# Kernel optimization log

Measured on AMD Instinct MI355X. Metric: run time of the kernel, lower is better.

The kernel has to match this reference:

```python
import jax, jax.numpy as jnp
import numpy as np

N_NODES = 100000
N_EDGES = 1600000
IN_CH = 128
HID_CH = 128
EMB_CH = 128
OUT_CH = 64


def _sage_conv(x, src, dst, W_l, b_l, W_r):
    # PyG SAGEConv (mean aggr): out = lin_l(mean_{j->i} x_j) + lin_r(x_i)
    n = x.shape[0]
    msg = x[src]                                             # [E, d] gather
    summed = jax.ops.segment_sum(msg, dst, num_segments=n)   # [N, d]
    cnt = jax.ops.segment_sum(jnp.ones((src.shape[0],), x.dtype), dst, num_segments=n)
    mean = summed / jnp.maximum(cnt, 1.0)[:, None]
    return mean @ W_l + b_l + x @ W_r


def setup_inputs() -> dict:
    key = jax.random.key(0)
    ks = jax.random.split(key, 10)
    x = jax.random.normal(ks[0], (N_NODES, IN_CH), dtype=jnp.float32)
    edge_index = jax.random.randint(ks[1], (2, N_EDGES), 0, N_NODES, dtype=jnp.int32)
    s1 = 1.0 / np.sqrt(IN_CH)
    s2 = 1.0 / np.sqrt(HID_CH)
    s3 = 1.0 / np.sqrt(EMB_CH)
    return {
        "x": x,
        "edge_index": edge_index,
        "W1l": jax.random.uniform(ks[2], (IN_CH, HID_CH), jnp.float32, -s1, s1),
        "b1": jnp.zeros((HID_CH,), jnp.float32),
        "W1r": jax.random.uniform(ks[3], (IN_CH, HID_CH), jnp.float32, -s1, s1),
        "W2l": jax.random.uniform(ks[4], (HID_CH, EMB_CH), jnp.float32, -s2, s2),
        "b2": jnp.zeros((EMB_CH,), jnp.float32),
        "W2r": jax.random.uniform(ks[5], (HID_CH, EMB_CH), jnp.float32, -s2, s2),
        "Wm": jax.random.uniform(ks[6], (EMB_CH, OUT_CH), jnp.float32, -s3, s3),
        "bm": jax.random.uniform(ks[7], (OUT_CH,), jnp.float32, -s3, s3),
    }


def reference(x, edge_index, W1l, b1, W1r, W2l, b2, W2r, Wm, bm):
    src, dst = edge_index[0], edge_index[1]
    h = jax.nn.relu(_sage_conv(x, src, dst, W1l, b1, W1r))
    emb = _sage_conv(h, src, dst, W2l, b2, W2r)
    out = emb @ Wm + bm
    # F.normalize(emb, p=2, dim=-1)
    norm = jnp.sqrt(jnp.sum(emb * emb, axis=-1, keepdims=True))
    emb_n = emb / jnp.maximum(norm, 1e-12)
    return out, emb_n
```

## Files before the change

### kernel.cpp

```cpp
#include <hip/hip_runtime.h>
#include <hip/hip_fp16.h>
#include <cstdint>
#include <cstddef>

#define N_NODES 100000
#define N_EDGES 1600000
#define BSH 6
#define BNODES 64
#define NB 1563
#define CHUNK 2048
#define LDK 136

typedef _Float16 f16x8 __attribute__((ext_vector_type(8)));
typedef float f32x4 __attribute__((ext_vector_type(4)));


__device__ __forceinline__ float h2f(ushort u) {
    __half_raw r;
    r.x = u;
    return __half2float(__half(r));
}

__device__ __forceinline__ ushort f2h(float f) {
    __half h = __float2half(f);
    return static_cast<__half_raw>(h).x;
}

__device__ __forceinline__ void acc4(float4& a, uint2 v) {
    a.x += h2f((ushort)(v.x & 0xffff));
    a.y += h2f((ushort)(v.x >> 16));
    a.z += h2f((ushort)(v.y & 0xffff));
    a.w += h2f((ushort)(v.y >> 16));
}


__global__ __launch_bounds__(256) void prep_all(
        const int* __restrict__ dst, int* __restrict__ bcnt, int E,
        const float* __restrict__ x, ushort* __restrict__ x_f16, int n4,
        const float* __restrict__ W1l, const float* __restrict__ W1r,
        const float* __restrict__ W2l, const float* __restrict__ W2r,
        const float* __restrict__ Wm,
        ushort* __restrict__ W1lP, ushort* __restrict__ W1rP,
        ushort* __restrict__ W2lP, ushort* __restrict__ W2rP,
        ushort* __restrict__ WmP) {
    int bid = blockIdx.x;
    if (bid < 256) {
        __shared__ int lh[NB];
        for (int i = threadIdx.x; i < NB; i += 256) lh[i] = 0;
        __syncthreads();
        for (int e = bid * 256 + threadIdx.x; e < E; e += 256 * 256)
            atomicAdd(&lh[dst[e] >> BSH], 1);
        __syncthreads();
        for (int i = threadIdx.x; i < NB; i += 256) {
            int v = lh[i];
            if (v) atomicAdd(&bcnt[i], v);
        }
    } else if (bid < 256 + 12500) {
        int i = (bid - 256) * 256 + threadIdx.x;
        if (i < n4) {
            float4 v = reinterpret_cast<const float4*>(x)[i];
            ushort4 o;
            o.x = f2h(v.x);
            o.y = f2h(v.y);
            o.z = f2h(v.z);
            o.w = f2h(v.w);
            reinterpret_cast<ushort4*>(x_f16)[i] = o;
        }
    } else {
        int t = (bid - (256 + 12500)) * 256 + threadIdx.x;
        if (t < 65536) {
            int wsel = t >> 14;
            int o = t & 16383;
            const float* srcs[4] = {W1l, W1r, W2l, W2r};
            ushort* dsts[4] = {W1lP, W1rP, W2lP, W2rP};
            int j = o & 7;
            int lane = (o >> 3) & 63;
            int kg = (o >> 9) & 3;
            int nf = o >> 11;
            int k = kg * 32 + (lane >> 4) * 8 + j;
            int c = nf * 16 + (lane & 15);
            dsts[wsel][o] = f2h(srcs[wsel][k * 128 + c]);
        } else if (t < 65536 + 8192) {
            int o = t - 65536;
            int j = o & 7;
            int lane = (o >> 3) & 63;
            int kg = (o >> 9) & 3;
            int nf = o >> 11;
            int k = kg * 32 + (lane >> 4) * 8 + j;
            int c = nf * 16 + (lane & 15);
            WmP[o] = f2h(Wm[k * 64 + c]);
        }
    }
}

__global__ void scan_buckets(const int* __restrict__ bcnt, int* __restrict__ boffs) {
    __shared__ int sdata[256];
    int tid = threadIdx.x;
    int v[8];
    int s = 0;
#pragma unroll
    for (int i = 0; i < 8; i++) {
        int idx = tid * 8 + i;
        v[i] = (idx < NB) ? bcnt[idx] : 0;
        s += v[i];
    }
    sdata[tid] = s;
    __syncthreads();
    int acc = s;
    for (int off = 1; off < 256; off <<= 1) {
        int t = (tid >= off) ? sdata[tid - off] : 0;
        __syncthreads();
        acc += t;
        sdata[tid] = acc;
        __syncthreads();
    }
    int excl = acc - s;
#pragma unroll
    for (int i = 0; i < 8; i++) {
        int idx = tid * 8 + i;
        if (idx < NB) boffs[idx] = excl;
        excl += v[i];
    }
}

__global__ void bucket_scatter(const int* __restrict__ src, const int* __restrict__ dst,
                               const int* __restrict__ boffs, int* __restrict__ gcur,
                               uint* __restrict__ bedges, int E) {
    __shared__ int lh[NB];
    __shared__ int lbase[NB];
    int nwg = gridDim.x;
    int chunk = (E + nwg - 1) / nwg;
    int e0 = blockIdx.x * chunk;
    int e1 = e0 + chunk;
    if (e1 > E) e1 = E;
    for (int i = threadIdx.x; i < NB; i += 256) lh[i] = 0;
    __syncthreads();
    for (int e = e0 + threadIdx.x; e < e1; e += 256)
        atomicAdd(&lh[dst[e] >> BSH], 1);
    __syncthreads();
    for (int i = threadIdx.x; i < NB; i += 256) {
        int v = lh[i];
        lbase[i] = v ? (boffs[i] + atomicAdd(&gcur[i], v)) : 0;
    }
    __syncthreads();
    for (int i = threadIdx.x; i < NB; i += 256) lh[i] = 0;
    __syncthreads();
    int e = e0 + threadIdx.x;
#pragma unroll 1
    for (; e + 3 * 256 < e1; e += 4 * 256) {
        int d0 = dst[e + 0 * 256], s0 = src[e + 0 * 256];
        int d1 = dst[e + 1 * 256], s1 = src[e + 1 * 256];
        int d2 = dst[e + 2 * 256], s2 = src[e + 2 * 256];
        int d3 = dst[e + 3 * 256], s3 = src[e + 3 * 256];
        int b0 = d0 >> BSH, b1 = d1 >> BSH, b2 = d2 >> BSH, b3 = d3 >> BSH;
        int r0 = atomicAdd(&lh[b0], 1);
        int r1 = atomicAdd(&lh[b1], 1);
        int r2 = atomicAdd(&lh[b2], 1);
        int r3 = atomicAdd(&lh[b3], 1);
        bedges[lbase[b0] + r0] = ((uint)(d0 & (BNODES - 1)) << 17) | (uint)s0;
        bedges[lbase[b1] + r1] = ((uint)(d1 & (BNODES - 1)) << 17) | (uint)s1;
        bedges[lbase[b2] + r2] = ((uint)(d2 & (BNODES - 1)) << 17) | (uint)s2;
        bedges[lbase[b3] + r3] = ((uint)(d3 & (BNODES - 1)) << 17) | (uint)s3;
    }
    for (; e < e1; e += 256) {
        int d = dst[e];
        int b = d >> BSH;
        int r = atomicAdd(&lh[b], 1);
        bedges[lbase[b] + r] = ((uint)(d & (BNODES - 1)) << 17) | (uint)src[e];
    }
}


__global__ __launch_bounds__(512) void aggregate_bucket(
        const ushort* __restrict__ F, const uint* __restrict__ bedges,
        const int* __restrict__ boffs, const int* __restrict__ bcnt,
        ushort* __restrict__ out, int n) {
    int b = blockIdx.x;
    int beg = boffs[b];
    int m = bcnt[b];
    int node0 = b << BSH;
    int nNodes = n - node0;
    if (nNodes > BNODES) nNodes = BNODES;
    __shared__ uint ls[CHUNK];
    __shared__ int lh[BNODES];
    __shared__ int lofs[BNODES];
    __shared__ int pcnt[BNODES];
    int tid = threadIdx.x;
    int wid = tid >> 6;
    int lane = tid & 63;
    int hw = lane >> 5;
    int cl = lane & 31;

    float4 acc[8];
#pragma unroll
    for (int i = 0; i < 8; i++) acc[i] = make_float4(0.f, 0.f, 0.f, 0.f);
    if (tid < BNODES) pcnt[tid] = 0;

    for (int base = 0; base < m; base += CHUNK) {
        int mm = m - base;
        if (mm > CHUNK) mm = CHUNK;
        __syncthreads();
        if (tid < BNODES) lh[tid] = 0;
        __syncthreads();
        for (int i = tid; i < mm; i += 512)
            atomicAdd(&lh[bedges[beg + base + i] >> 17], 1);
        __syncthreads();
        if (tid < BNODES) {
            int v = lh[tid];
            int s = v;
#pragma unroll
            for (int off = 1; off < 64; off <<= 1) {
                int t = __shfl_up(s, off);
                if (lane >= off) s += t;
            }
            lofs[tid] = s - v;
            pcnt[tid] += v;
            lh[tid] = 0;
        }
        __syncthreads();
        for (int i = tid; i < mm; i += 512) {
            uint p = bedges[beg + base + i];
            int k = p >> 17;
            int r = atomicAdd(&lh[k], 1);
            ls[lofs[k] + r] = p;
        }
        __syncthreads();
#pragma unroll
        for (int ki = 0; ki < 8; ki++) {
            int k = wid * 8 + ki;
            int s0 = lofs[k];
            int ck = lh[k];
            int j = hw;
            for (; j + 6 < ck; j += 8) {
                uint p0 = ls[s0 + j + 0] & 0x1FFFFu;
                uint p1 = ls[s0 + j + 2] & 0x1FFFFu;
                uint p2 = ls[s0 + j + 4] & 0x1FFFFu;
                uint p3 = ls[s0 + j + 6] & 0x1FFFFu;
                uint2 v0 = *reinterpret_cast<const uint2*>(F + (size_t)p0 * 128 + cl * 4);
                uint2 v1 = *reinterpret_cast<const uint2*>(F + (size_t)p1 * 128 + cl * 4);
                uint2 v2 = *reinterpret_cast<const uint2*>(F + (size_t)p2 * 128 + cl * 4);
                uint2 v3 = *reinterpret_cast<const uint2*>(F + (size_t)p3 * 128 + cl * 4);
                acc4(acc[ki], v0);
                acc4(acc[ki], v1);
                acc4(acc[ki], v2);
                acc4(acc[ki], v3);
            }
            for (; j < ck; j += 2) {
                uint p = ls[s0 + j] & 0x1FFFFu;
                uint2 v = *reinterpret_cast<const uint2*>(F + (size_t)p * 128 + cl * 4);
                acc4(acc[ki], v);
            }
        }
    }
    __syncthreads();
#pragma unroll
    for (int ki = 0; ki < 8; ki++) {
        acc[ki].x += __shfl_xor(acc[ki].x, 32);
        acc[ki].y += __shfl_xor(acc[ki].y, 32);
        acc[ki].z += __shfl_xor(acc[ki].z, 32);
        acc[ki].w += __shfl_xor(acc[ki].w, 32);
    }
    if (hw == 0) {
#pragma unroll
        for (int ki = 0; ki < 8; ki++) {
            int k = wid * 8 + ki;
            if (k < nNodes) {
                float inv = 1.0f / fmaxf((float)pcnt[k], 1.0f);
                uint2 o;
                o.x = (uint)f2h(acc[ki].x * inv) | ((uint)f2h(acc[ki].y * inv) << 16);
                o.y = (uint)f2h(acc[ki].z * inv) | ((uint)f2h(acc[ki].w * inv) << 16);
                *reinterpret_cast<uint2*>(out + (size_t)(node0 + k) * 128 + cl * 4) = o;
            }
        }
    }
}


__global__ __launch_bounds__(256) void gemm1(
        const ushort* __restrict__ A1, const ushort* __restrict__ W1lP,
        const ushort* __restrict__ A2, const ushort* __restrict__ W1rP,
        const float* __restrict__ b1, ushort* __restrict__ h_f16, int n) {
    __shared__ ushort ht[64 * LDK];
    int wid = threadIdx.x >> 6;
    int lane = threadIdx.x & 63;
    int row0 = blockIdx.x * 64 + wid * 16;
    int fr = lane & 15;
    int ko = (lane >> 4) * 8;
    int arow = row0 + fr;
    if (arow >= n) arow = n - 1;

    f32x4 acc[8];
#pragma unroll
    for (int nf = 0; nf < 8; nf++) acc[nf] = (f32x4)0.f;

    for (int seg = 0; seg < 2; ++seg) {
        const ushort* A = seg ? A2 : A1;
        const ushort* WP = seg ? W1rP : W1lP;
#pragma unroll
        for (int kg = 0; kg < 4; kg++) {
            f16x8 av = *reinterpret_cast<const f16x8*>(A + (size_t)arow * 128 + kg * 32 + ko);
#pragma unroll
            for (int nf = 0; nf < 8; nf++) {
                f16x8 bv = *reinterpret_cast<const f16x8*>(WP + (nf * 4 + kg) * 512 + lane * 8);
                acc[nf] = __builtin_amdgcn_mfma_f32_16x16x32_f16(av, bv, acc[nf], 0, 0, 0);
            }
        }
    }

    int crow = (lane >> 4) * 4;
    int ccol = lane & 15;
#pragma unroll
    for (int reg = 0; reg < 4; reg++) {
        int lrow = wid * 16 + crow + reg;
#pragma unroll
        for (int nf = 0; nf < 8; nf++) {
            float v = acc[nf][reg] + b1[nf * 16 + ccol];
            v = fmaxf(v, 0.f);
            ht[lrow * LDK + nf * 16 + ccol] = f2h(v);
        }
    }
    __syncthreads();

#pragma unroll
    for (int i = 0; i < 16; i++) {
        int row = wid * 16 + i;
        int grow = blockIdx.x * 64 + row;
        if (grow < n) {
            reinterpret_cast<uint*>(h_f16 + (size_t)grow * 128)[lane] =
                reinterpret_cast<const uint*>(&ht[row * LDK])[lane];
        }
    }
}


__global__ __launch_bounds__(256) void gemm2(
        const ushort* __restrict__ A1, const ushort* __restrict__ W2lP,
        const ushort* __restrict__ A2, const ushort* __restrict__ W2rP,
        const float* __restrict__ b2, const ushort* __restrict__ WmP,
        const float* __restrict__ bm, float* __restrict__ outp,
        float* __restrict__ embn, int n) {
    __shared__ ushort et[64 * LDK];
    __shared__ float rnorm[64];
    int wid = threadIdx.x >> 6;
    int lane = threadIdx.x & 63;
    int row0 = blockIdx.x * 64 + wid * 16;
    int fr = lane & 15;
    int ko = (lane >> 4) * 8;
    int arow = row0 + fr;
    if (arow >= n) arow = n - 1;

    f32x4 acc[8];
#pragma unroll
    for (int nf = 0; nf < 8; nf++) acc[nf] = (f32x4)0.f;

    for (int seg = 0; seg < 2; ++seg) {
        const ushort* A = seg ? A2 : A1;
        const ushort* WP = seg ? W2rP : W2lP;
#pragma unroll
        for (int kg = 0; kg < 4; kg++) {
            f16x8 av = *reinterpret_cast<const f16x8*>(A + (size_t)arow * 128 + kg * 32 + ko);
#pragma unroll
            for (int nf = 0; nf < 8; nf++) {
                f16x8 bv = *reinterpret_cast<const f16x8*>(WP + (nf * 4 + kg) * 512 + lane * 8);
                acc[nf] = __builtin_amdgcn_mfma_f32_16x16x32_f16(av, bv, acc[nf], 0, 0, 0);
            }
        }
    }

    int crow = (lane >> 4) * 4;
    int ccol = lane & 15;
#pragma unroll
    for (int reg = 0; reg < 4; reg++) {
        float vv[8];
        float ss = 0.f;
#pragma unroll
        for (int nf = 0; nf < 8; nf++) {
            float v = acc[nf][reg] + b2[nf * 16 + ccol];
            vv[nf] = v;
            ss += v * v;
        }
        ss += __shfl_xor(ss, 1);
        ss += __shfl_xor(ss, 2);
        ss += __shfl_xor(ss, 4);
        ss += __shfl_xor(ss, 8);
        float inv = 1.0f / fmaxf(sqrtf(ss), 1e-12f);
        int lrow = wid * 16 + crow + reg;
#pragma unroll
        for (int nf = 0; nf < 8; nf++)
            et[lrow * LDK + nf * 16 + ccol] = f2h(vv[nf]);
        if (ccol == 0) rnorm[lrow] = inv;
    }
    __syncthreads();

#pragma unroll
    for (int i = 0; i < 16; i++) {
        int row = wid * 16 + i;
        int grow = blockIdx.x * 64 + row;
        if (grow < n) {
            float inv = rnorm[row];
            ushort2 e = reinterpret_cast<const ushort2*>(&et[row * LDK])[lane];
            float2 o;
            o.x = h2f(e.x) * inv;
            o.y = h2f(e.y) * inv;
            reinterpret_cast<float2*>(embn + (size_t)grow * 128)[lane] = o;
        }
    }

    f32x4 acc2[4];
#pragma unroll
    for (int nf = 0; nf < 4; nf++) acc2[nf] = (f32x4)0.f;
#pragma unroll
    for (int kg = 0; kg < 4; kg++) {
        f16x8 av = *reinterpret_cast<const f16x8*>(&et[(wid * 16 + fr) * LDK + kg * 32 + ko]);
#pragma unroll
        for (int nf = 0; nf < 4; nf++) {
            f16x8 bv = *reinterpret_cast<const f16x8*>(WmP + (nf * 4 + kg) * 512 + lane * 8);
            acc2[nf] = __builtin_amdgcn_mfma_f32_16x16x32_f16(av, bv, acc2[nf], 0, 0, 0);
        }
    }
#pragma unroll
    for (int reg = 0; reg < 4; reg++) {
        int grow = row0 + crow + reg;
        if (grow < n) {
#pragma unroll
            for (int nf = 0; nf < 4; nf++)
                outp[(size_t)grow * 64 + nf * 16 + ccol] = acc2[nf][reg] + bm[nf * 16 + ccol];
        }
    }
}


extern "C" void kernel_launch(void* const* d_in, const int* in_sizes, int n_in,
                              void* d_out, int out_size, void* d_ws, size_t ws_size,
                              hipStream_t stream) {
    const float* x   = (const float*)d_in[0];
    const int*   ei  = (const int*)d_in[1];
    const float* W1l = (const float*)d_in[2];
    const float* b1  = (const float*)d_in[3];
    const float* W1r = (const float*)d_in[4];
    const float* W2l = (const float*)d_in[5];
    const float* b2  = (const float*)d_in[6];
    const float* W2r = (const float*)d_in[7];
    const float* Wm  = (const float*)d_in[8];
    const float* bm  = (const float*)d_in[9];

    const int N = N_NODES, E = N_EDGES;
    const int* src = ei;
    const int* dst = ei + E;

    char* ws = (char*)d_ws;
    int* bcnt  = (int*)ws;  ws += sizeof(int) * NB;
    int* boffs = (int*)ws;  ws += sizeof(int) * NB;
    int* gcur  = (int*)ws;  ws += sizeof(int) * NB;
    uintptr_t p0 = ((uintptr_t)ws + 255) & ~(uintptr_t)255;
    uint* bedges = (uint*)p0;
    uintptr_t p1 = ((uintptr_t)(bedges + N_EDGES) + 255) & ~(uintptr_t)255;
    ushort* mean_f16 = (ushort*)p1;
    ushort* x_f16    = mean_f16 + (size_t)N * 128;
    ushort* h_f16    = x_f16 + (size_t)N * 128;
    ushort* W1lP     = h_f16 + (size_t)N * 128;
    ushort* W1rP     = W1lP + 128 * 128;
    ushort* W2lP     = W1rP + 128 * 128;
    ushort* W2rP     = W2lP + 128 * 128;
    ushort* WmP      = W2rP + 128 * 128;

    float* outp = (float*)d_out;
    float* embn = outp + (size_t)N * 64;

    hipMemsetAsync(bcnt, 0, sizeof(int) * NB, stream);
    hipMemsetAsync(gcur, 0, sizeof(int) * NB, stream);

    int n4 = N * 128 / 4;
    int prep_blocks = 256 + 12500 + 288;
    prep_all<<<prep_blocks, 256, 0, stream>>>(dst, bcnt, E, x, x_f16, n4,
                                              W1l, W1r, W2l, W2r, Wm,
                                              W1lP, W1rP, W2lP, W2rP, WmP);
    scan_buckets<<<1, 256, 0, stream>>>(bcnt, boffs);
    bucket_scatter<<<256, 256, 0, stream>>>(src, dst, boffs, gcur, bedges, E);

    int gblk = (N + 63) / 64;

    aggregate_bucket<<<NB, 512, 0, stream>>>(x_f16, bedges, boffs, bcnt, mean_f16, N);
    gemm1<<<gblk, 256, 0, stream>>>(mean_f16, W1lP, x_f16, W1rP, b1, h_f16, N);

    aggregate_bucket<<<NB, 512, 0, stream>>>(h_f16, bedges, boffs, bcnt, mean_f16, N);
    gemm2<<<gblk, 256, 0, stream>>>(mean_f16, W2lP, h_f16, W2rP, b2,
                                    WmP, bm, outp, embn, N);
}
```

Baseline: 287.9 us.

## Presort edges into per-node CSR once and aggregate with feature-sliced blocks

Adds a sort_buckets kernel that turns the bucketed edge list into a per-node CSR (sorted sources, offsets, counts) once, so both aggregation passes reuse it instead of re-sorting each bucket in shared memory. The aggregation kernel now splits the 128 features into four 32-column slices, one block per slice, with 16-lane groups reading 4-byte pieces. This removes the repeated in-block histogram, atomics and syncs and raises block count, but each source row is now fetched as four narrow 64-byte pieces spread across four blocks, and it adds an extra kernel plus workspace.

```diff
diff --git a/kernel.cpp b/kernel.cpp
--- a/kernel.cpp
+++ b/kernel.cpp
@@ -8,7 +8,6 @@
 #define BSH 6
 #define BNODES 64
 #define NB 1563
-#define CHUNK 2048
 #define LDK 136
 
 typedef _Float16 f16x8 __attribute__((ext_vector_type(8)));
@@ -24,13 +23,6 @@
 __device__ __forceinline__ ushort f2h(float f) {
     __half h = __float2half(f);
     return static_cast<__half_raw>(h).x;
-}
-
-__device__ __forceinline__ void acc4(float4& a, uint2 v) {
-    a.x += h2f((ushort)(v.x & 0xffff));
-    a.y += h2f((ushort)(v.x >> 16));
-    a.z += h2f((ushort)(v.y & 0xffff));
-    a.w += h2f((ushort)(v.y >> 16));
 }
 
 
@@ -171,106 +163,89 @@
 }
 
 
-__global__ __launch_bounds__(512) void aggregate_bucket(
-        const ushort* __restrict__ F, const uint* __restrict__ bedges,
-        const int* __restrict__ boffs, const int* __restrict__ bcnt,
-        ushort* __restrict__ out, int n) {
+__global__ __launch_bounds__(256) void sort_buckets(
+        const uint* __restrict__ bedges, const int* __restrict__ boffs,
+        const int* __restrict__ bcnt, uint* __restrict__ srcs_sorted,
+        int* __restrict__ noffs, int* __restrict__ ncnt, int n) {
+    __shared__ int lh[BNODES];
+    __shared__ int lofs[BNODES];
     int b = blockIdx.x;
     int beg = boffs[b];
     int m = bcnt[b];
     int node0 = b << BSH;
-    int nNodes = n - node0;
-    if (nNodes > BNODES) nNodes = BNODES;
-    __shared__ uint ls[CHUNK];
-    __shared__ int lh[BNODES];
-    __shared__ int lofs[BNODES];
-    __shared__ int pcnt[BNODES];
     int tid = threadIdx.x;
-    int wid = tid >> 6;
-    int lane = tid & 63;
-    int hw = lane >> 5;
-    int cl = lane & 31;
-
-    float4 acc[8];
-#pragma unroll
-    for (int i = 0; i < 8; i++) acc[i] = make_float4(0.f, 0.f, 0.f, 0.f);
-    if (tid < BNODES) pcnt[tid] = 0;
-
-    for (int base = 0; base < m; base += CHUNK) {
-        int mm = m - base;
-        if (mm > CHUNK) mm = CHUNK;
-        __syncthreads();
-        if (tid < BNODES) lh[tid] = 0;
-        __syncthreads();
-        for (int i = tid; i < mm; i += 512)
-            atomicAdd(&lh[bedges[beg + base + i] >> 17], 1);
-        __syncthreads();
-        if (tid < BNODES) {
-            int v = lh[tid];
-            int s = v;
-#pragma unroll
-            for (int off = 1; off < 64; off <<= 1) {
-                int t = __shfl_up(s, off);
-                if (lane >= off) s += t;
-            }
-            lofs[tid] = s - v;
-            pcnt[tid] += v;
-            lh[tid] = 0;
-        }
-        __syncthreads();
-        for (int i = tid; i < mm; i += 512) {
-            uint p = bedges[beg + base + i];
-            int k = p >> 17;
-            int r = atomicAdd(&lh[k], 1);
-            ls[lofs[k] + r] = p;
-        }
-        __syncthreads();
-#pragma unroll
-        for (int ki = 0; ki < 8; ki++) {
-            int k = wid * 8 + ki;
-            int s0 = lofs[k];
-            int ck = lh[k];
-            int j = hw;
-            for (; j + 6 < ck; j += 8) {
-                uint p0 = ls[s0 + j + 0] & 0x1FFFFu;
-                uint p1 = ls[s0 + j + 2] & 0x1FFFFu;
-                uint p2 = ls[s0 + j + 4] & 0x1FFFFu;
-                uint p3 = ls[s0 + j + 6] & 0x1FFFFu;
-                uint2 v0 = *reinterpret_cast<const uint2*>(F + (size_t)p0 * 128 + cl * 4);
-                uint2 v1 = *reinterpret_cast<const uint2*>(F + (size_t)p1 * 128 + cl * 4);
-                uint2 v2 = *reinterpret_cast<const uint2*>(F + (size_t)p2 * 128 + cl * 4);
-                uint2 v3 = *reinterpret_cast<const uint2*>(F + (size_t)p3 * 128 + cl * 4);
-                acc4(acc[ki], v0);
-                acc4(acc[ki], v1);
-                acc4(acc[ki], v2);
-                acc4(acc[ki], v3);
-            }
-            for (; j < ck; j += 2) {
-                uint p = ls[s0 + j] & 0x1FFFFu;
-                uint2 v = *reinterpret_cast<const uint2*>(F + (size_t)p * 128 + cl * 4);
-                acc4(acc[ki], v);
-            }
-        }
-    }
-    __syncthreads();
-#pragma unroll
-    for (int ki = 0; ki < 8; ki++) {
-        acc[ki].x += __shfl_xor(acc[ki].x, 32);
-        acc[ki].y += __shfl_xor(acc[ki].y, 32);
-        acc[ki].z += __shfl_xor(acc[ki].z, 32);
-        acc[ki].w += __shfl_xor(acc[ki].w, 32);
-    }
-    if (hw == 0) {
-#pragma unroll
-        for (int ki = 0; ki < 8; ki++) {
-            int k = wid * 8 + ki;
-            if (k < nNodes) {
-                float inv = 1.0f / fmaxf((float)pcnt[k], 1.0f);
-                uint2 o;
-                o.x = (uint)f2h(acc[ki].x * inv) | ((uint)f2h(acc[ki].y * inv) << 16);
-                o.y = (uint)f2h(acc[ki].z * inv) | ((uint)f2h(acc[ki].w * inv) << 16);
-                *reinterpret_cast<uint2*>(out + (size_t)(node0 + k) * 128 + cl * 4) = o;
-            }
+    if (tid < BNODES) lh[tid] = 0;
+    __syncthreads();
+    for (int i = tid; i < m; i += 256)
+        atomicAdd(&lh[bedges[beg + i] >> 17], 1);
+    __syncthreads();
+    if (tid < BNODES) {
+        int v = lh[tid];
+        int s = v;
+#pragma unroll
+        for (int off = 1; off < 64; off <<= 1) {
+            int t = __shfl_up(s, off);
+            if (tid >= off) s += t;
+        }
+        lofs[tid] = s - v;
+        if (node0 + tid < n) {
+            noffs[node0 + tid] = beg + s - v;
+            ncnt[node0 + tid] = v;
+        }
+        lh[tid] = 0;
+    }
+    __syncthreads();
+    for (int i = tid; i < m; i += 256) {
+        uint p = bedges[beg + i];
+        int k = p >> 17;
+        int r = atomicAdd(&lh[k], 1);
+        srcs_sorted[beg + lofs[k] + r] = p & 0x1FFFFu;
+    }
+}
+
+
+__global__ __launch_bounds__(256) void aggregate_sliced(
+        const ushort* __restrict__ F, const uint* __restrict__ srcs,
+        const int* __restrict__ noffs, const int* __restrict__ ncnt,
+        ushort* __restrict__ out, int n) {
+    int bi = blockIdx.x;
+    int b = bi >> 2;
+    int s = bi & 3;
+    int w = threadIdx.x >> 6;
+    int lane = threadIdx.x & 63;
+    int g = lane >> 4;
+    int cl = lane & 15;
+    const ushort* Fs = F + s * 32 + cl * 2;
+#pragma unroll 1
+    for (int ki = 0; ki < 16; ki++) {
+        int node = (b << BSH) + w * 16 + ki;
+        if (node >= n) continue;
+        int o = noffs[node];
+        int c = ncnt[node];
+        float ax = 0.f, ay = 0.f;
+        int j = g;
+        for (; j + 4 < c; j += 8) {
+            uint s0 = srcs[o + j];
+            uint s1 = srcs[o + j + 4];
+            uint v0 = *reinterpret_cast<const uint*>(Fs + (size_t)s0 * 128);
+            uint v1 = *reinterpret_cast<const uint*>(Fs + (size_t)s1 * 128);
+            ax += h2f((ushort)(v0 & 0xffff)) + h2f((ushort)(v1 & 0xffff));
+            ay += h2f((ushort)(v0 >> 16)) + h2f((ushort)(v1 >> 16));
+        }
+        if (j < c) {
+            uint s0 = srcs[o + j];
+            uint v0 = *reinterpret_cast<const uint*>(Fs + (size_t)s0 * 128);
+            ax += h2f((ushort)(v0 & 0xffff));
+            ay += h2f((ushort)(v0 >> 16));
+        }
+        ax += __shfl_xor(ax, 16);
+        ay += __shfl_xor(ay, 16);
+        ax += __shfl_xor(ax, 32);
+        ay += __shfl_xor(ay, 32);
+        if (g == 0) {
+            float inv = 1.0f / fmaxf((float)c, 1.0f);
+            uint o2 = (uint)f2h(ax * inv) | ((uint)f2h(ay * inv) << 16);
+            *reinterpret_cast<uint*>(out + (size_t)node * 128 + s * 32 + cl * 2) = o2;
         }
     }
 }
@@ -452,9 +427,12 @@
     int* bcnt  = (int*)ws;  ws += sizeof(int) * NB;
     int* boffs = (int*)ws;  ws += sizeof(int) * NB;
     int* gcur  = (int*)ws;  ws += sizeof(int) * NB;
+    int* noffs = (int*)ws;  ws += sizeof(int) * N_NODES;
+    int* ncnt  = (int*)ws;  ws += sizeof(int) * N_NODES;
     uintptr_t p0 = ((uintptr_t)ws + 255) & ~(uintptr_t)255;
     uint* bedges = (uint*)p0;
-    uintptr_t p1 = ((uintptr_t)(bedges + N_EDGES) + 255) & ~(uintptr_t)255;
+    uint* srcs_sorted = bedges + N_EDGES;
+    uintptr_t p1 = ((uintptr_t)(srcs_sorted + N_EDGES) + 255) & ~(uintptr_t)255;
     ushort* mean_f16 = (ushort*)p1;
     ushort* x_f16    = mean_f16 + (size_t)N * 128;
     ushort* h_f16    = x_f16 + (size_t)N * 128;
@@ -477,13 +455,17 @@
                                               W1lP, W1rP, W2lP, W2rP, WmP);
     scan_buckets<<<1, 256, 0, stream>>>(bcnt, boffs);
     bucket_scatter<<<256, 256, 0, stream>>>(src, dst, boffs, gcur, bedges, E);
+    sort_buckets<<<NB, 256, 0, stream>>>(bedges, boffs, bcnt,
+                                         srcs_sorted, noffs, ncnt, N);
 
     int gblk = (N + 63) / 64;
 
-    aggregate_bucket<<<NB, 512, 0, stream>>>(x_f16, bedges, boffs, bcnt, mean_f16, N);
+    aggregate_sliced<<<NB * 4, 256, 0, stream>>>(x_f16, srcs_sorted, noffs, ncnt,
+                                                 mean_f16, N);
     gemm1<<<gblk, 256, 0, stream>>>(mean_f16, W1lP, x_f16, W1rP, b1, h_f16, N);
 
-    aggregate_bucket<<<NB, 512, 0, stream>>>(h_f16, bedges, boffs, bcnt, mean_f16, N);
+    aggregate_sliced<<<NB * 4, 256, 0, stream>>>(h_f16, srcs_sorted, noffs, ncnt,
+                                                 mean_f16, N);
     gemm2<<<gblk, 256, 0, stream>>>(mean_f16, W2lP, h_f16, W2rP, b2,
                                     WmP, bm, outp, embn, N);
 }
```

After: 444.1 us. +54.2%, slower.
